# Kernel tuning notes

Hardware: AMD Instinct MI355X
Metric: run time of the kernel (lower is better)

## Reference

```python
import jax, jax.numpy as jnp
import numpy as np

NUM_HEADS = 16
D_HEAD = 128
D_MODEL = NUM_HEADS * D_HEAD  # 2048
D_LATENT = 512
F8 = jnp.float8_e4m3fn


def _q8(a):
    # emulate fp8 e4m3 numerics: quantize then compute in fp32
    return a.astype(F8).astype(jnp.float32)


def setup_inputs() -> dict:
    key = jax.random.key(0)
    ks = jax.random.split(key, 12)
    B, S = 8, 8192
    s = 0.02
    return {
        "x": jax.random.normal(ks[0], (B, S, D_MODEL), jnp.float32),
        "Wq": jax.random.normal(ks[1], (D_MODEL, D_MODEL), jnp.float32) * s,
        "bq": jnp.zeros((D_MODEL,), jnp.float32),
        "Wkv_down": jax.random.normal(ks[2], (D_MODEL, 2 * D_LATENT), jnp.float32) * s,
        "bkv_down": jnp.zeros((2 * D_LATENT,), jnp.float32),
        "Wq_down": jax.random.normal(ks[3], (D_MODEL, D_LATENT), jnp.float32) * s,
        "bq_down": jnp.zeros((D_LATENT,), jnp.float32),
        "Wkv_up": jax.random.normal(ks[4], (D_LATENT, 2 * D_MODEL), jnp.float32) * s,
        "bkv_up": jnp.zeros((2 * D_MODEL,), jnp.float32),
        "Wout": jax.random.normal(ks[5], (D_MODEL, D_MODEL), jnp.float32) * s,
        "bout": jnp.zeros((D_MODEL,), jnp.float32),
        "top_k": 2048,
    }


def reference(x, Wq, bq, Wkv_down, bkv_down, Wq_down, bq_down, Wkv_up, bkv_up, Wout, bout, top_k):
    B, S, D = x.shape
    # low-rank MQA KV cache projection: [B, S, d_latent] each
    KV = x @ Wkv_down + bkv_down
    K_down, V_down = jnp.split(KV, 2, axis=-1)

    # ---- lightning indexer (fp8-emulated fuzzy scores for the last query) ----
    q_last = x[:, -1, :]                                  # [B, D]
    q_idx = _q8(q_last) @ _q8(Wq_down) + _q8(bq_down)     # [B, d_latent]
    scores = jax.nn.relu(jnp.einsum("bl,bsl->bs", q_idx, _q8(K_down)))  # [B, S]
    _, idx = jax.lax.top_k(scores, top_k)                 # [B, k]

    # gather selected low-rank K/V tokens: [B, k, d_latent]
    K_sel = jnp.take_along_axis(K_down, idx[:, :, None], axis=1)
    V_sel = jnp.take_along_axis(V_down, idx[:, :, None], axis=1)

    # up-project to full width and split heads: [B, k, H, d_head]
    Wk_up, Wv_up = jnp.split(Wkv_up, 2, axis=1)
    bk_up, bv_up = jnp.split(bkv_up, 2, axis=0)
    K = (K_sel @ Wk_up + bk_up).reshape(B, top_k, NUM_HEADS, D_HEAD)
    V = (V_sel @ Wv_up + bv_up).reshape(B, top_k, NUM_HEADS, D_HEAD)

    # query for the current (last) position: [B, H, d_head]
    q = (q_last @ Wq + bq).reshape(B, NUM_HEADS, D_HEAD)

    logits = jnp.einsum("bhd,bkhd->bhk", q, K) / np.float32(np.sqrt(D_HEAD))
    attn = jax.nn.softmax(logits, axis=-1)                # [B, H, k]
    o = jnp.einsum("bhk,bkhd->bhd", attn, V).reshape(B, D)
    return o @ Wout + bout                                # [B, d_model]
```

## Files before the change

kernel.cpp:

```cpp
#include <hip/hip_runtime.h>
#include <hip/hip_bf16.h>
#include <math.h>

#define B_ 8
#define S_ 8192
#define D_ 2048
#define L_ 512
#define H_ 16
#define DH_ 128
#define TOPK_ 2048
#define EXTCAP 24
#define SLOTS (TOPK_ + 64)
#define RCAP 131072
#define DELTA 6e-6f
#define QCH 32
#define QCHD (D_ / QCH)
#define PCH 8
#define PCHD (D_ / PCH)
#define VCH 8
#define VCHK (SLOTS / VCH)

typedef __attribute__((ext_vector_type(8))) short short8;
typedef __attribute__((ext_vector_type(4))) float f32x4;

__device__ __forceinline__ float q8(float x) {
  float ax = fabsf(x);
  if (!(ax >= 0.015625f)) return rintf(x * 512.0f) * 0.001953125f;
  int ee; frexpf(ax, &ee);
  float step = ldexpf(1.0f, ee - 4);
  return rintf(ldexpf(x, 4 - ee)) * step;
}

__device__ __forceinline__ float q8_midf(float v, float* qflip, float* dist) {
  float av = fabsf(v);
  float step, u;
  if (!(av >= 0.015625f)) { step = 0.001953125f; u = v * 512.0f; }
  else { int ee; frexpf(av, &ee); step = ldexpf(1.0f, ee - 4); u = ldexpf(v, 4 - ee); }
  float m = rintf(u);
  float f = u - m;
  *dist = (0.5f - fabsf(f)) * step;
  float sgn = (f >= 0.0f) ? 1.0f : -1.0f;
  *qflip = (m + sgn) * step;
  return m * step;
}

__device__ __forceinline__ float b2f(unsigned u) {
  return __uint_as_float(u << 16);
}

__device__ __forceinline__ ushort bfr(float x) {
  unsigned u = __float_as_uint(x);
  return (ushort)((u + 0x7FFFu + ((u >> 16) & 1u)) >> 16);
}
__device__ __forceinline__ float uf(ushort h) {
  return __uint_as_float(((unsigned)h) << 16);
}
__device__ __forceinline__ void split3(float x, ushort& h, ushort& m, ushort& l) {
  h = bfr(x); float r = x - uf(h);
  m = bfr(r); float r2 = r - uf(m);
  l = bfr(r2);
}

__device__ __forceinline__ f32x4 mfma16(short8 a, short8 b, f32x4 c) {
  return __builtin_amdgcn_mfma_f32_16x16x32_bf16(a, b, c, 0, 0, 0);
}

#if __has_builtin(__builtin_amdgcn_global_load_lds)
#define HAS_GLL 1
__device__ __forceinline__ void gload_lds16(const void* g, void* l) {
  __builtin_amdgcn_global_load_lds(
      (const __attribute__((address_space(1))) void*)g,
      (__attribute__((address_space(3))) void*)l, 16, 0, 0);
}
#else
#define HAS_GLL 0
#endif

__global__ __launch_bounds__(256) void zero_kernel(
    int* flag, int* riskyCnt, int* extraCnt, int* cntI2O) {
  int i = blockIdx.x * 256 + threadIdx.x;
  if (i < B_ * S_) flag[i] = 0;
  if (i == 0) *riskyCnt = 0;
  if (i < B_) { extraCnt[i] = 0; cntI2O[i] = 0; }
}

__global__ __launch_bounds__(256) void wsplit_kernel(
    const float* __restrict__ W, ushort* __restrict__ Wsp) {
  const int c = blockIdx.x * 256 + threadIdx.x;
  const int kblk = blockIdx.y;
  float xe[32];
#pragma unroll
  for (int e = 0; e < 32; ++e) xe[e] = W[(long)(kblk * 32 + e) * 1024 + c];
#pragma unroll
  for (int kb = 0; kb < 4; ++kb) {
    ushort Hh[8], Mm[8], Ll[8];
#pragma unroll
    for (int e = 0; e < 8; ++e) split3(xe[kb * 8 + e], Hh[e], Mm[e], Ll[e]);
    *(short8*)&Wsp[((((long)0 * 64 + kblk) * 4 + kb) * 1024 + c) * 8] = *(short8*)Hh;
    *(short8*)&Wsp[((((long)1 * 64 + kblk) * 4 + kb) * 1024 + c) * 8] = *(short8*)Mm;
    *(short8*)&Wsp[((((long)2 * 64 + kblk) * 4 + kb) * 1024 + c) * 8] = *(short8*)Ll;
  }
}

__global__ __launch_bounds__(256) void wq8_kernel(
    const float* __restrict__ Wqd, ushort* __restrict__ Wq8) {
  const long i = ((long)blockIdx.x * 256 + threadIdx.x) * 4;
  float4 v = *(const float4*)(Wqd + i);
  ushort4 o;
  o.x = (ushort)(__float_as_uint(q8(v.x)) >> 16);
  o.y = (ushort)(__float_as_uint(q8(v.y)) >> 16);
  o.z = (ushort)(__float_as_uint(q8(v.z)) >> 16);
  o.w = (ushort)(__float_as_uint(q8(v.w)) >> 16);
  *(ushort4*)(Wq8 + i) = o;
}

#define AS_IDX(T, kb, r) ((((T)*4 + (kb)) * 128 + (r)) * 8)
#define BS_IDX(T, kb, n) ((((T)*4 + (kb)) * 128 + (n)) * 8)

template <bool QUANT>
__global__ __launch_bounds__(256, 2) void gemm_mfma(
    const float* __restrict__ X, const ushort* __restrict__ Wsp, int colbase,
    int mbase, const float* __restrict__ bias, float* __restrict__ C,
    ushort* __restrict__ Cq8, const int* __restrict__ rowmap,
    int2* __restrict__ riskyList, int* __restrict__ riskyCnt) {
  __shared__ __align__(16) ushort As[3 * 4 * 128 * 8];
  __shared__ __align__(16) ushort Bs[3 * 4 * 128 * 8];
  const int tid = threadIdx.x;
  const int m0 = (mbase + blockIdx.y) * 128;
  const int n0 = blockIdx.x * 128;
  const int ar_ = tid >> 1;
  const int kh = (tid & 1) << 4;
  const int arow = rowmap ? rowmap[m0 + ar_] : (m0 + ar_);
  const float* aptr = X + (long)arow * D_ + kh;
  const int cb = colbase + n0;

  f32x4 acc[4][4];
#pragma unroll
  for (int i = 0; i < 4; ++i)
#pragma unroll
    for (int j = 0; j < 4; ++j) acc[i][j] = (f32x4){0.f, 0.f, 0.f, 0.f};

  const int w = tid >> 6, lane = tid & 63;
  const int wm = (w & 1) * 64, wn = (w >> 1) * 64;
  const int lr = lane & 15, lq = lane >> 4;

  float4 v0 = *(const float4*)(aptr + 0);
  float4 v1 = *(const float4*)(aptr + 4);
  float4 v2 = *(const float4*)(aptr + 8);
  float4 v3 = *(const float4*)(aptr + 12);

  for (int k0 = 0; k0 < D_; k0 += 32) {
    const int kblk = k0 >> 5;

    __syncthreads();

#pragma unroll
    for (int i = 0; i < 6; ++i) {
      const int c = w * 6 + i;
      const int s = c >> 1, half = c & 1;
      const int T = s >> 2, kb = s & 3;
      const ushort* g = Wsp + ((((long)T * 64 + kblk) * 4 + kb) * 1024 +
                               (long)cb + half * 64 + lane) * 8;
#if HAS_GLL
      gload_lds16(g, &Bs[(s * 128 + half * 64) * 8]);
#else
      *(short8*)&Bs[(s * 128 + half * 64 + lane) * 8] = *(const short8*)g;
#endif
    }

    {
      float xe[16] = {v0.x, v0.y, v0.z, v0.w, v1.x, v1.y, v1.z, v1.w,
                      v2.x, v2.y, v2.z, v2.w, v3.x, v3.y, v3.z, v3.w};
      const int kb0 = (tid & 1) * 2;
#pragma unroll
      for (int j8 = 0; j8 < 2; ++j8) {
        ushort Hh[8], Mm[8], Ll[8];
#pragma unroll
        for (int e = 0; e < 8; ++e) split3(xe[j8 * 8 + e], Hh[e], Mm[e], Ll[e]);
        *(short8*)&As[AS_IDX(0, kb0 + j8, ar_)] = *(short8*)Hh;
        *(short8*)&As[AS_IDX(1, kb0 + j8, ar_)] = *(short8*)Mm;
        *(short8*)&As[AS_IDX(2, kb0 + j8, ar_)] = *(short8*)Ll;
      }
    }
    if (k0 + 32 < D_) {
      v0 = *(const float4*)(aptr + k0 + 32);
      v1 = *(const float4*)(aptr + k0 + 36);
      v2 = *(const float4*)(aptr + k0 + 40);
      v3 = *(const float4*)(aptr + k0 + 44);
    }
    __syncthreads();

    short8 af[4][3];
#pragma unroll
    for (int mf = 0; mf < 4; ++mf)
#pragma unroll
      for (int T = 0; T < 3; ++T)
        af[mf][T] = *(const short8*)&As[AS_IDX(T, lq, wm + mf * 16 + lr)];
#pragma unroll
    for (int nf = 0; nf < 4; ++nf) {
      short8 bh = *(const short8*)&Bs[BS_IDX(0, lq, wn + nf * 16 + lr)];
      short8 bm = *(const short8*)&Bs[BS_IDX(1, lq, wn + nf * 16 + lr)];
      short8 bl = *(const short8*)&Bs[BS_IDX(2, lq, wn + nf * 16 + lr)];
#pragma unroll
      for (int mf = 0; mf < 4; ++mf) {
        f32x4 c = acc[mf][nf];
        c = mfma16(af[mf][0], bh, c);
        c = mfma16(af[mf][0], bm, c);
        c = mfma16(af[mf][1], bh, c);
        c = mfma16(af[mf][0], bl, c);
        c = mfma16(af[mf][2], bh, c);
        c = mfma16(af[mf][1], bm, c);
        acc[mf][nf] = c;
      }
    }
  }

#pragma unroll
  for (int nf = 0; nf < 4; ++nf) {
    const int ng = n0 + wn + nf * 16 + lr;
    const float bb = bias[ng];
#pragma unroll
    for (int mf = 0; mf < 4; ++mf) {
      const int mg = m0 + wm + mf * 16 + lq * 4;
#pragma unroll
      for (int i = 0; i < 4; ++i) {
        float v = acc[mf][nf][i] + bb;
        const long crow = (long)(mg + i);
        C[crow * L_ + ng] = v;
        if (QUANT) {
          float qflip, dist;
          float q = q8_midf(v, &qflip, &dist);
          Cq8[crow * L_ + ng] = (ushort)(__float_as_uint(q) >> 16);
          if (dist < DELTA) {
            int idx = atomicAdd(riskyCnt, 1);
            if (idx < RCAP) {
              unsigned qbits = __float_as_uint(qflip) >> 16;
              riskyList[idx] = make_int2((int)crow, (ng << 16) | (int)qbits);
            }
          }
        }
      }
    }
  }
}

__global__ __launch_bounds__(256) void qidx_part(
    const float* __restrict__ x, const ushort* __restrict__ Wq8,
    double* __restrict__ qpart) {
  __shared__ float qs[QCHD];
  const int b = blockIdx.y;
  const int c = blockIdx.x;
  const int t = threadIdx.x;
  const int d0 = c * QCHD;
  const float* xr = x + ((long)b * S_ + (S_ - 1)) * D_ + d0;
  if (t < QCHD) qs[t] = q8(xr[t]);
  __syncthreads();
  double a0 = 0.0, a1 = 0.0;
  const ushort* wr = Wq8 + (long)d0 * L_;
  for (int dd = 0; dd < QCHD; ++dd) {
    const double qv = (double)qs[dd];
    a0 += qv * (double)b2f((unsigned)wr[dd * L_ + t]);
    a1 += qv * (double)b2f((unsigned)wr[dd * L_ + t + 256]);
  }
  double* qp = qpart + ((long)b * QCH + c) * L_;
  qp[t] = a0;
  qp[t + 256] = a1;
}

__global__ __launch_bounds__(256) void qidx_reduce(
    const double* __restrict__ qpart, const float* __restrict__ bqd,
    float* __restrict__ qidx) {
  const int i = blockIdx.x * 256 + threadIdx.x;
  const int b = i >> 9, l = i & 511;
  double acc = 0.0;
  for (int c = 0; c < QCH; ++c)
    acc += qpart[((long)b * QCH + c) * L_ + l];
  qidx[i] = (float)(acc + (double)q8(bqd[l]));
}

__global__ __launch_bounds__(256) void scores_kernel(
    const ushort* __restrict__ Kq8, const float* __restrict__ qidx,
    float* __restrict__ scores) {
  __shared__ float qs[L_];
  const int m0 = blockIdx.x * 4;
  const int b = m0 >> 13;
  const int t = threadIdx.x;
  if (t < 128) ((float4*)qs)[t] = ((const float4*)(qidx + b * L_))[t];
  __syncthreads();
  const int wave = t >> 6, lane = t & 63;
  const long m = m0 + wave;
  uint4 rv = *(const uint4*)(Kq8 + m * L_ + lane * 8);
  const float* q = qs + lane * 8;
  float p = 0.f;
  p = fmaf(q[0], b2f(rv.x & 0xffffu), p);
  p = fmaf(q[1], b2f(rv.x >> 16), p);
  p = fmaf(q[2], b2f(rv.y & 0xffffu), p);
  p = fmaf(q[3], b2f(rv.y >> 16), p);
  p = fmaf(q[4], b2f(rv.z & 0xffffu), p);
  p = fmaf(q[5], b2f(rv.z >> 16), p);
  p = fmaf(q[6], b2f(rv.w & 0xffffu), p);
  p = fmaf(q[7], b2f(rv.w >> 16), p);
#pragma unroll
  for (int off = 32; off >= 1; off >>= 1) p += __shfl_xor(p, off, 64);
  if (lane == 0) scores[m] = (p > 0.f) ? p : 0.f;
}

__global__ __launch_bounds__(256) void topk_kernel(
    const float* __restrict__ scores, int* __restrict__ rowmap,
    float* __restrict__ vstarF) {
  __shared__ unsigned su[S_];
  __shared__ int red[256];
  __shared__ int cgt_sh;
  const int b = blockIdx.x, t = threadIdx.x;
  const int wave = t >> 6, lane = t & 63;
  for (int i = t; i < S_; i += 256) su[i] = __float_as_uint(scores[(long)b * S_ + i]);
  __syncthreads();
  unsigned prefix = 0u;
  for (int bit = 30; bit >= 0; --bit) {
    unsigned cand = prefix | (1u << bit);
    int c = 0;
    for (int i = t; i < S_; i += 256) c += (su[i] >= cand) ? 1 : 0;
#pragma unroll
    for (int off = 32; off >= 1; off >>= 1) c += __shfl_xor(c, off, 64);
    if (lane == 0) red[wave] = c;
    __syncthreads();
    int total = red[0] + red[1] + red[2] + red[3];
    if (total >= TOPK_) prefix = cand;
    __syncthreads();
  }
  const unsigned vstar = prefix;
  if (t == 0) vstarF[b] = __uint_as_float(vstar);
  const int c0 = t * 32;
  int cnt = 0;
  for (int i = 0; i < 32; ++i) cnt += (su[c0 + i] > vstar) ? 1 : 0;
  red[t] = cnt;
  __syncthreads();
  if (t == 0) {
    int run = 0;
    for (int i = 0; i < 256; ++i) { int c = red[i]; red[i] = run; run += c; }
    cgt_sh = run;
  }
  __syncthreads();
  int pos = red[t];
  for (int i = 0; i < 32; ++i)
    if (su[c0 + i] > vstar) rowmap[b * TOPK_ + pos++] = b * S_ + c0 + i;
  __syncthreads();
  int tcnt = 0;
  for (int i = 0; i < 32; ++i) tcnt += (su[c0 + i] == vstar) ? 1 : 0;
  red[t] = tcnt;
  __syncthreads();
  if (t == 0) {
    int run = 0;
    for (int i = 0; i < 256; ++i) { int c = red[i]; red[i] = run; run += c; }
  }
  __syncthreads();
  int tpos = cgt_sh + red[t];
  for (int i = 0; i < 32; ++i)
    if (su[c0 + i] == vstar) {
      if (tpos < TOPK_) rowmap[b * TOPK_ + tpos] = b * S_ + c0 + i;
      ++tpos;
    }
}

__global__ __launch_bounds__(256) void risky_eval(
    const int2* __restrict__ list, const int* __restrict__ riskyCnt,
    const ushort* __restrict__ Kq8, const float* __restrict__ qidx,
    const float* __restrict__ scores, const float* __restrict__ vstarF,
    int* __restrict__ flag, int* __restrict__ extraRows,
    int* __restrict__ extraCnt, int* __restrict__ cntI2O) {
  int i = blockIdx.x * 256 + threadIdx.x;
  int n = min(*riskyCnt, RCAP);
  if (i >= n) return;
  int row = list[i].x;
  int l = list[i].y >> 16;
  float qflip = b2f((unsigned)(list[i].y & 0xffff));
  int b = row >> 13;
  float qorig = b2f((unsigned)Kq8[(long)row * L_ + l]);
  float shift = qidx[b * L_ + l] * (qflip - qorig);
  float s = scores[row];
  float vs = vstarF[b];
  bool in0 = (s >= vs);
  bool in1 = (s + shift >= vs);
  if (in0 != in1) {
    if (atomicCAS(&flag[row], 0, 1) == 0) {
      if (in0) {
        atomicAdd(&cntI2O[b], 1);
      } else {
        int e = atomicAdd(&extraCnt[b], 1);
        if (e < EXTCAP) extraRows[b * EXTCAP + e] = row;
      }
    }
  }
}

__global__ __launch_bounds__(256) void counterparty_kernel(
    const float* __restrict__ scores, const int* __restrict__ rowmap,
    const float* __restrict__ vstarF, int* __restrict__ flag,
    int* __restrict__ extraRows, int* __restrict__ extraCnt,
    const int* __restrict__ cntI2O) {
  __shared__ float bv[256];
  __shared__ int bi[256];
  const int b = blockIdx.x, t = threadIdx.x;
  const float vs = vstarF[b];
  const int nA = min(extraCnt[b], EXTCAP);
  const int nD = min(cntI2O[b], EXTCAP);
  for (int pass = 0; pass < nA; ++pass) {
    float best = 3.4e38f; int besti = -1;
    for (int k = t; k < TOPK_; k += 256) {
      int r = rowmap[b * TOPK_ + k];
      if (!flag[r]) { float s = scores[r]; if (s < best) { best = s; besti = r; } }
    }
    bv[t] = best; bi[t] = besti; __syncthreads();
    for (int off = 128; off > 0; off >>= 1) {
      if (t < off && bv[t + off] < bv[t]) { bv[t] = bv[t + off]; bi[t] = bi[t + off]; }
      __syncthreads();
    }
    if (t == 0 && bi[0] >= 0) flag[bi[0]] = 1;
    __syncthreads();
  }
  for (int pass = 0; pass < nD; ++pass) {
    float best = -3.4e38f; int besti = -1;
    for (int s0 = t; s0 < S_; s0 += 256) {
      int r = b * S_ + s0;
      float s = scores[r];
      if (s < vs && !flag[r] && s > best) { best = s; besti = r; }
    }
    bv[t] = best; bi[t] = besti; __syncthreads();
    for (int off = 128; off > 0; off >>= 1) {
      if (t < off && bv[t + off] > bv[t]) { bv[t] = bv[t + off]; bi[t] = bi[t + off]; }
      __syncthreads();
    }
    if (t == 0 && bi[0] >= 0) {
      flag[bi[0]] = 1;
      int e = extraCnt[b];
      if (e < EXTCAP) { extraRows[b * EXTCAP + e] = bi[0]; extraCnt[b] = e + 1; }
    }
    __syncthreads();
  }
}

__global__ __launch_bounds__(256) void buildext_kernel(
    const int* __restrict__ rowmap, const int* __restrict__ extraRows,
    const int* __restrict__ extraCnt, const int* __restrict__ flag,
    int* __restrict__ rowmapExt, float* __restrict__ multExt) {
  const int b = blockIdx.y;
  const int k = blockIdx.x * 256 + threadIdx.x;
  if (k >= SLOTS) return;
  const int tot = min(extraCnt[b], EXTCAP);
  int row; float m;
  if (k < TOPK_) { row = rowmap[b * TOPK_ + k]; m = flag[row] ? 0.5f : 1.0f; }
  else if (k - TOPK_ < tot) { row = extraRows[b * EXTCAP + (k - TOPK_)]; m = 0.5f; }
  else { row = b * S_; m = 0.0f; }
  rowmapExt[b * SLOTS + k] = row;
  multExt[b * SLOTS + k] = m;
}

__global__ __launch_bounds__(128) void qproj_part(
    const float* __restrict__ x, const float* __restrict__ Wq,
    float* __restrict__ ppart) {
  __shared__ float xs[PCHD];
  const int b = blockIdx.y, c = blockIdx.z, t = threadIdx.x;
  const int d0 = c * PCHD;
  const float* xr = x + ((long)b * S_ + (S_ - 1)) * D_ + d0;
  xs[t] = xr[t]; xs[t + 128] = xr[t + 128];
  __syncthreads();
  const int n = blockIdx.x * 128 + t;
  float acc = 0.f;
  for (int dd = 0; dd < PCHD; ++dd)
    acc = fmaf(xs[dd], Wq[(long)(d0 + dd) * D_ + n], acc);
  ppart[((long)c * B_ + b) * D_ + n] = acc;
}

__global__ __launch_bounds__(256) void qproj_reduce(
    const float* __restrict__ ppart, const float* __restrict__ bq,
    float* __restrict__ q) {
  const int i = blockIdx.x * 256 + threadIdx.x;
  const int b = i >> 11, n = i & (D_ - 1);
  float acc = 0.f;
  for (int c = 0; c < PCH; ++c)
    acc += ppart[((long)c * B_ + b) * D_ + n];
  q[i] = acc + bq[n];
}

__global__ __launch_bounds__(256) void qt_kernel(
    const float* __restrict__ q, const float* __restrict__ Wkvu,
    const float* __restrict__ bkvu, float* __restrict__ qt,
    float* __restrict__ blog) {
  __shared__ float qh[DH_];
  __shared__ float red[DH_];
  const int h = blockIdx.x, b = blockIdx.y, t = threadIdx.x;
  if (t < DH_) qh[t] = q[b * D_ + h * DH_ + t];
  __syncthreads();
  for (int l = t; l < L_; l += 256) {
    const float* wr = Wkvu + (long)l * 4096 + h * DH_;
    float acc = 0.f;
    for (int d = 0; d < DH_; d += 4) {
      float4 w4 = *(const float4*)(wr + d);
      acc = fmaf(qh[d], w4.x, acc);
      acc = fmaf(qh[d + 1], w4.y, acc);
      acc = fmaf(qh[d + 2], w4.z, acc);
      acc = fmaf(qh[d + 3], w4.w, acc);
    }
    qt[((long)b * H_ + h) * L_ + l] = acc;
  }
  if (t < DH_) red[t] = qh[t] * bkvu[h * DH_ + t];
  __syncthreads();
  if (t == 0) {
    float s = 0.f;
    for (int i = 0; i < DH_; ++i) s += red[i];
    blog[b * H_ + h] = s;
  }
}

__global__ __launch_bounds__(256) void logits_kernel(
    const float* __restrict__ Kd, const int* __restrict__ rowmapExt,
    const float* __restrict__ qt, const float* __restrict__ blog,
    float* __restrict__ logits) {
  const int b = blockIdx.y;
  const int k = blockIdx.x * 16 + (threadIdx.x >> 4);
  const int h = threadIdx.x & 15;
  const float* kr = Kd + (long)rowmapExt[b * SLOTS + k] * L_;
  const float* qr = qt + ((long)b * H_ + h) * L_;
  float acc = 0.f;
  for (int l = 0; l < L_; l += 4) {
    float4 kv = *(const float4*)(kr + l);
    acc = fmaf(qr[l], kv.x, acc);
    acc = fmaf(qr[l + 1], kv.y, acc);
    acc = fmaf(qr[l + 2], kv.z, acc);
    acc = fmaf(qr[l + 3], kv.w, acc);
  }
  logits[((long)b * H_ + h) * SLOTS + k] =
      (acc + blog[b * H_ + h]) * 0.088388347648318447f;
}

__global__ __launch_bounds__(256) void softmax_kernel(
    float* __restrict__ logits, const float* __restrict__ multExt) {
  __shared__ float redf[4];
  __shared__ double redd[4];
  const int bh = blockIdx.x;
  const int b = bh >> 4;
  float* row = logits + (long)bh * SLOTS;
  const float* mult = multExt + b * SLOTS;
  const int t = threadIdx.x;
  const int wave = t >> 6, lane = t & 63;
  float m = -3.4e38f;
  for (int i = t; i < SLOTS; i += 256) m = fmaxf(m, row[i]);
#pragma unroll
  for (int off = 32; off >= 1; off >>= 1) m = fmaxf(m, __shfl_xor(m, off, 64));
  if (lane == 0) redf[wave] = m;
  __syncthreads();
  m = fmaxf(fmaxf(redf[0], redf[1]), fmaxf(redf[2], redf[3]));
  double s = 0.0;
  for (int i = t; i < SLOTS; i += 256) {
    float e = expf(row[i] - m) * mult[i];
    row[i] = e;
    s += (double)e;
  }
#pragma unroll
  for (int off = 32; off >= 1; off >>= 1) s += __shfl_xor(s, off, 64);
  if (lane == 0) redd[wave] = s;
  __syncthreads();
  const float inv = (float)(1.0 / (redd[0] + redd[1] + redd[2] + redd[3]));
  for (int i = t; i < SLOTS; i += 256) row[i] *= inv;
}

__global__ __launch_bounds__(256) void vt_part(
    const float* __restrict__ Vsel, const float* __restrict__ attn,
    float* __restrict__ vpart) {
  const int b = blockIdx.y, c = blockIdx.z;
  const int t = threadIdx.x;
  const int l = blockIdx.x * 64 + (t & 63);
  const int hg = t >> 6;
  float acc[4] = {0.f, 0.f, 0.f, 0.f};
  const float* ar = attn + (long)b * H_ * SLOTS;
  const int k0 = c * VCHK, k1 = k0 + VCHK;
  for (int k = k0; k < k1; ++k) {
    float v = Vsel[((long)b * SLOTS + k) * L_ + l];
#pragma unroll
    for (int a = 0; a < 4; ++a)
      acc[a] = fmaf(ar[(hg * 4 + a) * SLOTS + k], v, acc[a]);
  }
#pragma unroll
  for (int a = 0; a < 4; ++a)
    vpart[(((long)c * B_ + b) * H_ + hg * 4 + a) * L_ + l] = acc[a];
}

__global__ __launch_bounds__(256) void vt_reduce(
    const float* __restrict__ vpart, float* __restrict__ vt) {
  const int i = blockIdx.x * 256 + threadIdx.x;
  float acc = 0.f;
  for (int c = 0; c < VCH; ++c)
    acc += vpart[(long)c * (B_ * H_ * L_) + i];
  vt[i] = acc;
}

__global__ __launch_bounds__(128) void oproj_kernel(
    const float* __restrict__ vt, const float* __restrict__ Wkvu,
    const float* __restrict__ bkvu, float* __restrict__ o) {
  __shared__ float vs[L_];
  const int h = blockIdx.x, b = blockIdx.y, t = threadIdx.x;
  for (int i = t; i < L_ / 4; i += 128)
    ((float4*)vs)[i] = ((const float4*)(vt + ((long)b * H_ + h) * L_))[i];
  __syncthreads();
  const int col = h * DH_ + t;
  float acc = 0.f;
  for (int l = 0; l < L_; ++l)
    acc = fmaf(vs[l], Wkvu[(long)l * 4096 + 2048 + col], acc);
  o[b * D_ + col] = acc + bkvu[2048 + col];
}

__global__ __launch_bounds__(128) void out_part(
    const float* __restrict__ o, const float* __restrict__ Wout,
    float* __restrict__ opart) {
  __shared__ float os[PCHD];
  const int b = blockIdx.y, c = blockIdx.z, t = threadIdx.x;
  const int d0 = c * PCHD;
  const float* orr = o + (long)b * D_ + d0;
  os[t] = orr[t]; os[t + 128] = orr[t + 128];
  __syncthreads();
  const int n = blockIdx.x * 128 + t;
  float acc = 0.f;
  for (int dd = 0; dd < PCHD; ++dd)
    acc = fmaf(os[dd], Wout[(long)(d0 + dd) * D_ + n], acc);
  opart[((long)c * B_ + b) * D_ + n] = acc;
}

__global__ __launch_bounds__(256) void out_reduce(
    const float* __restrict__ opart, const float* __restrict__ bout,
    float* __restrict__ out) {
  const int i = blockIdx.x * 256 + threadIdx.x;
  const int b = i >> 11, n = i & (D_ - 1);
  float acc = 0.f;
  for (int c = 0; c < PCH; ++c)
    acc += opart[((long)c * B_ + b) * D_ + n];
  out[i] = acc + bout[n];
}

extern "C" void kernel_launch(void* const* d_in, const int* in_sizes, int n_in,
                              void* d_out, int out_size, void* d_ws, size_t ws_size,
                              hipStream_t stream) {
  const float* x    = (const float*)d_in[0];
  const float* Wq   = (const float*)d_in[1];
  const float* bq   = (const float*)d_in[2];
  const float* Wkvd = (const float*)d_in[3];
  const float* bkvd = (const float*)d_in[4];
  const float* Wqd  = (const float*)d_in[5];
  const float* bqd  = (const float*)d_in[6];
  const float* Wkvu = (const float*)d_in[7];
  const float* bkvu = (const float*)d_in[8];
  const float* Wo   = (const float*)d_in[9];
  const float* bo   = (const float*)d_in[10];
  float* out = (float*)d_out;

  char* p = (char*)d_ws;
  auto alloc = [&](size_t bytes) {
    char* r = p;
    p += (bytes + 255) & ~(size_t)255;
    return r;
  };
  float*  Kd       = (float*)alloc((size_t)B_ * S_ * L_ * 4);
  ushort* Kq8      = (ushort*)alloc((size_t)B_ * S_ * L_ * 2);
  float*  Vsel     = (float*)alloc((size_t)B_ * SLOTS * L_ * 4);
  ushort* Wsp      = (ushort*)alloc((size_t)3 * 64 * 4 * 1024 * 8 * 2);
  ushort* Wq8      = (ushort*)alloc((size_t)D_ * L_ * 2);
  double* qpart    = (double*)alloc((size_t)B_ * QCH * L_ * 8);
  float*  ppart    = (float*)alloc((size_t)PCH * B_ * D_ * 4);
  float*  opart    = (float*)alloc((size_t)PCH * B_ * D_ * 4);
  float*  vpart    = (float*)alloc((size_t)VCH * B_ * H_ * L_ * 4);
  float*  scores   = (float*)alloc((size_t)B_ * S_ * 4);
  float*  qidx     = (float*)alloc((size_t)B_ * L_ * 4);
  int*    rowmap   = (int*)alloc((size_t)B_ * TOPK_ * 4);
  int*    rowmapE  = (int*)alloc((size_t)B_ * SLOTS * 4);
  float*  multE    = (float*)alloc((size_t)B_ * SLOTS * 4);
  float*  vstarF   = (float*)alloc((size_t)B_ * 4);
  int2*   riskyL   = (int2*)alloc((size_t)RCAP * 8);
  int*    riskyCnt = (int*)alloc(256);
  int*    flagArr  = (int*)alloc((size_t)B_ * S_ * 4);
  int*    extraR   = (int*)alloc((size_t)B_ * EXTCAP * 4);
  int*    extraCnt = (int*)alloc((size_t)B_ * 4);
  int*    cntI2O   = (int*)alloc((size_t)B_ * 4);
  float*  qv       = (float*)alloc((size_t)B_ * D_ * 4);
  float*  qt       = (float*)alloc((size_t)B_ * H_ * L_ * 4);
  float*  blog     = (float*)alloc((size_t)B_ * H_ * 4);
  float*  logits   = (float*)alloc((size_t)B_ * H_ * SLOTS * 4);
  float*  vt       = (float*)alloc((size_t)B_ * H_ * L_ * 4);
  float*  ov       = (float*)alloc((size_t)B_ * D_ * 4);
  (void)ws_size; (void)in_sizes; (void)n_in; (void)out_size;

  zero_kernel<<<(B_ * S_ + 255) / 256, 256, 0, stream>>>(flagArr, riskyCnt, extraCnt, cntI2O);
  wsplit_kernel<<<dim3(4, 64), 256, 0, stream>>>(Wkvd, Wsp);
  wq8_kernel<<<(D_ * L_ / 4) / 256, 256, 0, stream>>>(Wqd, Wq8);
  gemm_mfma<true><<<dim3(4, 256), 256, 0, stream>>>(
      x, Wsp, 0, 0, bkvd, Kd, Kq8, nullptr, riskyL, riskyCnt);
  gemm_mfma<true><<<dim3(4, 256), 256, 0, stream>>>(
      x, Wsp, 0, 256, bkvd, Kd, Kq8, nullptr, riskyL, riskyCnt);
  qidx_part<<<dim3(QCH, B_), 256, 0, stream>>>(x, Wq8, qpart);
  qidx_reduce<<<(B_ * L_) / 256, 256, 0, stream>>>(qpart, bqd, qidx);
  scores_kernel<<<(B_ * S_) / 4, 256, 0, stream>>>(Kq8, qidx, scores);
  topk_kernel<<<B_, 256, 0, stream>>>(scores, rowmap, vstarF);
  risky_eval<<<RCAP / 256, 256, 0, stream>>>(riskyL, riskyCnt, Kq8, qidx, scores, vstarF,
                                             flagArr, extraR, extraCnt, cntI2O);
  counterparty_kernel<<<B_, 256, 0, stream>>>(scores, rowmap, vstarF, flagArr, extraR, extraCnt, cntI2O);
  buildext_kernel<<<dim3((SLOTS + 255) / 256, B_), 256, 0, stream>>>(rowmap, extraR, extraCnt, flagArr, rowmapE, multE);
  gemm_mfma<false><<<dim3(4, (B_ * SLOTS) / 128), 256, 0, stream>>>(
      x, Wsp, 512, 0, bkvd + 512, Vsel, nullptr, rowmapE, nullptr, nullptr);
  qproj_part<<<dim3(D_ / 128, B_, PCH), 128, 0, stream>>>(x, Wq, ppart);
  qproj_reduce<<<(B_ * D_) / 256, 256, 0, stream>>>(ppart, bq, qv);
  qt_kernel<<<dim3(H_, B_), 256, 0, stream>>>(qv, Wkvu, bkvu, qt, blog);
  logits_kernel<<<dim3(SLOTS / 16, B_), 256, 0, stream>>>(Kd, rowmapE, qt, blog, logits);
  softmax_kernel<<<B_ * H_, 256, 0, stream>>>(logits, multE);
  vt_part<<<dim3(L_ / 64, B_, VCH), 256, 0, stream>>>(Vsel, logits, vpart);
  vt_reduce<<<(B_ * H_ * L_) / 256, 256, 0, stream>>>(vpart, vt);
  oproj_kernel<<<dim3(H_, B_), 128, 0, stream>>>(vt, Wkvu, bkvu, ov);
  out_part<<<dim3(D_ / 128, B_, PCH), 128, 0, stream>>>(ov, Wo, opart);
  out_reduce<<<(B_ * D_) / 256, 256, 0, stream>>>(opart, bo, out);
}
```

Measured before the change: 1.597 ms.

## Cut V-gather GEMM to two-term split, remap blocks, register topk, split oproj

The V-selection GEMM now uses only the high/mid bf16 split terms (three MFMAs instead of six per fragment) and skips loading and storing the low term. GEMM blocks are remapped from a 1D grid so consecutive blocks land on different XCDs. topk keeps its 32 scores per thread in registers instead of shared memory. oproj splits the latent reduction across 512 threads. The reduced-precision V path lowers accuracy of the selected V projections, which may push error past tolerance.

```diff
diff --git a/kernel.cpp b/kernel.cpp
--- a/kernel.cpp
+++ b/kernel.cpp
@@ -117,17 +117,20 @@
 #define AS_IDX(T, kb, r) ((((T)*4 + (kb)) * 128 + (r)) * 8)
 #define BS_IDX(T, kb, n) ((((T)*4 + (kb)) * 128 + (n)) * 8)
 
-template <bool QUANT>
+template <bool QUANT, int NT>
 __global__ __launch_bounds__(256, 2) void gemm_mfma(
     const float* __restrict__ X, const ushort* __restrict__ Wsp, int colbase,
     int mbase, const float* __restrict__ bias, float* __restrict__ C,
     ushort* __restrict__ Cq8, const int* __restrict__ rowmap,
     int2* __restrict__ riskyList, int* __restrict__ riskyCnt) {
+  constexpr int NP = (NT == 6) ? 3 : 2;
   __shared__ __align__(16) ushort As[3 * 4 * 128 * 8];
   __shared__ __align__(16) ushort Bs[3 * 4 * 128 * 8];
   const int tid = threadIdx.x;
-  const int m0 = (mbase + blockIdx.y) * 128;
-  const int n0 = blockIdx.x * 128;
+  const int cpx = gridDim.x >> 3;
+  const int lid = (blockIdx.x & 7) * cpx + (blockIdx.x >> 3);
+  const int m0 = (mbase + (lid >> 2)) * 128;
+  const int n0 = (lid & 3) * 128;
   const int ar_ = tid >> 1;
   const int kh = (tid & 1) << 4;
   const int arow = rowmap ? rowmap[m0 + ar_] : (m0 + ar_);
@@ -154,9 +157,10 @@
 
     __syncthreads();
 
-#pragma unroll
-    for (int i = 0; i < 6; ++i) {
-      const int c = w * 6 + i;
+    constexpr int CHW = NP * 2;
+#pragma unroll
+    for (int i = 0; i < CHW; ++i) {
+      const int c = w * CHW + i;
       const int s = c >> 1, half = c & 1;
       const int T = s >> 2, kb = s & 3;
       const ushort* g = Wsp + ((((long)T * 64 + kblk) * 4 + kb) * 1024 +
@@ -179,7 +183,8 @@
         for (int e = 0; e < 8; ++e) split3(xe[j8 * 8 + e], Hh[e], Mm[e], Ll[e]);
         *(short8*)&As[AS_IDX(0, kb0 + j8, ar_)] = *(short8*)Hh;
         *(short8*)&As[AS_IDX(1, kb0 + j8, ar_)] = *(short8*)Mm;
-        *(short8*)&As[AS_IDX(2, kb0 + j8, ar_)] = *(short8*)Ll;
+        if (NP == 3)
+          *(short8*)&As[AS_IDX(2, kb0 + j8, ar_)] = *(short8*)Ll;
       }
     }
     if (k0 + 32 < D_) {
@@ -192,24 +197,29 @@
 
     short8 af[4][3];
 #pragma unroll
-    for (int mf = 0; mf < 4; ++mf)
-#pragma unroll
-      for (int T = 0; T < 3; ++T)
-        af[mf][T] = *(const short8*)&As[AS_IDX(T, lq, wm + mf * 16 + lr)];
+    for (int mf = 0; mf < 4; ++mf) {
+      af[mf][0] = *(const short8*)&As[AS_IDX(0, lq, wm + mf * 16 + lr)];
+      af[mf][1] = *(const short8*)&As[AS_IDX(1, lq, wm + mf * 16 + lr)];
+      if (NP == 3)
+        af[mf][2] = *(const short8*)&As[AS_IDX(2, lq, wm + mf * 16 + lr)];
+    }
 #pragma unroll
     for (int nf = 0; nf < 4; ++nf) {
       short8 bh = *(const short8*)&Bs[BS_IDX(0, lq, wn + nf * 16 + lr)];
       short8 bm = *(const short8*)&Bs[BS_IDX(1, lq, wn + nf * 16 + lr)];
-      short8 bl = *(const short8*)&Bs[BS_IDX(2, lq, wn + nf * 16 + lr)];
+      short8 bl;
+      if (NP == 3) bl = *(const short8*)&Bs[BS_IDX(2, lq, wn + nf * 16 + lr)];
 #pragma unroll
       for (int mf = 0; mf < 4; ++mf) {
         f32x4 c = acc[mf][nf];
         c = mfma16(af[mf][0], bh, c);
         c = mfma16(af[mf][0], bm, c);
         c = mfma16(af[mf][1], bh, c);
-        c = mfma16(af[mf][0], bl, c);
-        c = mfma16(af[mf][2], bh, c);
-        c = mfma16(af[mf][1], bm, c);
+        if (NT == 6) {
+          c = mfma16(af[mf][0], bl, c);
+          c = mfma16(af[mf][2], bh, c);
+          c = mfma16(af[mf][1], bm, c);
+        }
         acc[mf][nf] = c;
       }
     }
@@ -308,18 +318,21 @@
 __global__ __launch_bounds__(256) void topk_kernel(
     const float* __restrict__ scores, int* __restrict__ rowmap,
     float* __restrict__ vstarF) {
-  __shared__ unsigned su[S_];
   __shared__ int red[256];
   __shared__ int cgt_sh;
   const int b = blockIdx.x, t = threadIdx.x;
   const int wave = t >> 6, lane = t & 63;
-  for (int i = t; i < S_; i += 256) su[i] = __float_as_uint(scores[(long)b * S_ + i]);
-  __syncthreads();
+  const int c0 = t * 32;
+  unsigned sv[32];
+#pragma unroll
+  for (int i = 0; i < 32; ++i)
+    sv[i] = __float_as_uint(scores[(long)b * S_ + c0 + i]);
   unsigned prefix = 0u;
   for (int bit = 30; bit >= 0; --bit) {
     unsigned cand = prefix | (1u << bit);
     int c = 0;
-    for (int i = t; i < S_; i += 256) c += (su[i] >= cand) ? 1 : 0;
+#pragma unroll
+    for (int i = 0; i < 32; ++i) c += (sv[i] >= cand) ? 1 : 0;
 #pragma unroll
     for (int off = 32; off >= 1; off >>= 1) c += __shfl_xor(c, off, 64);
     if (lane == 0) red[wave] = c;
@@ -330,9 +343,9 @@
   }
   const unsigned vstar = prefix;
   if (t == 0) vstarF[b] = __uint_as_float(vstar);
-  const int c0 = t * 32;
   int cnt = 0;
-  for (int i = 0; i < 32; ++i) cnt += (su[c0 + i] > vstar) ? 1 : 0;
+#pragma unroll
+  for (int i = 0; i < 32; ++i) cnt += (sv[i] > vstar) ? 1 : 0;
   red[t] = cnt;
   __syncthreads();
   if (t == 0) {
@@ -342,11 +355,13 @@
   }
   __syncthreads();
   int pos = red[t];
+#pragma unroll
   for (int i = 0; i < 32; ++i)
-    if (su[c0 + i] > vstar) rowmap[b * TOPK_ + pos++] = b * S_ + c0 + i;
+    if (sv[i] > vstar) rowmap[b * TOPK_ + pos++] = b * S_ + c0 + i;
   __syncthreads();
   int tcnt = 0;
-  for (int i = 0; i < 32; ++i) tcnt += (su[c0 + i] == vstar) ? 1 : 0;
+#pragma unroll
+  for (int i = 0; i < 32; ++i) tcnt += (sv[i] == vstar) ? 1 : 0;
   red[t] = tcnt;
   __syncthreads();
   if (t == 0) {
@@ -355,8 +370,9 @@
   }
   __syncthreads();
   int tpos = cgt_sh + red[t];
+#pragma unroll
   for (int i = 0; i < 32; ++i)
-    if (su[c0 + i] == vstar) {
+    if (sv[i] == vstar) {
       if (tpos < TOPK_) rowmap[b * TOPK_ + tpos] = b * S_ + c0 + i;
       ++tpos;
     }
@@ -594,19 +610,27 @@
   vt[i] = acc;
 }
 
-__global__ __launch_bounds__(128) void oproj_kernel(
+__global__ __launch_bounds__(512) void oproj_kernel(
     const float* __restrict__ vt, const float* __restrict__ Wkvu,
     const float* __restrict__ bkvu, float* __restrict__ o) {
   __shared__ float vs[L_];
+  __shared__ float part[4][DH_];
   const int h = blockIdx.x, b = blockIdx.y, t = threadIdx.x;
-  for (int i = t; i < L_ / 4; i += 128)
-    ((float4*)vs)[i] = ((const float4*)(vt + ((long)b * H_ + h) * L_))[i];
-  __syncthreads();
-  const int col = h * DH_ + t;
+  if (t < 128)
+    ((float4*)vs)[t] = ((const float4*)(vt + ((long)b * H_ + h) * L_))[t];
+  __syncthreads();
+  const int lc = t >> 7;
+  const int ct = t & 127;
+  const int col = h * DH_ + ct;
   float acc = 0.f;
-  for (int l = 0; l < L_; ++l)
+  const int l0 = lc * 128;
+  for (int l = l0; l < l0 + 128; ++l)
     acc = fmaf(vs[l], Wkvu[(long)l * 4096 + 2048 + col], acc);
-  o[b * D_ + col] = acc + bkvu[2048 + col];
+  part[lc][ct] = acc;
+  __syncthreads();
+  if (lc == 0)
+    o[b * D_ + col] = ((part[0][ct] + part[1][ct]) + (part[2][ct] + part[3][ct]))
+                      + bkvu[2048 + col];
 }
 
 __global__ __launch_bounds__(128) void out_part(
@@ -690,9 +714,9 @@
   zero_kernel<<<(B_ * S_ + 255) / 256, 256, 0, stream>>>(flagArr, riskyCnt, extraCnt, cntI2O);
   wsplit_kernel<<<dim3(4, 64), 256, 0, stream>>>(Wkvd, Wsp);
   wq8_kernel<<<(D_ * L_ / 4) / 256, 256, 0, stream>>>(Wqd, Wq8);
-  gemm_mfma<true><<<dim3(4, 256), 256, 0, stream>>>(
+  gemm_mfma<true, 6><<<1024, 256, 0, stream>>>(
       x, Wsp, 0, 0, bkvd, Kd, Kq8, nullptr, riskyL, riskyCnt);
-  gemm_mfma<true><<<dim3(4, 256), 256, 0, stream>>>(
+  gemm_mfma<true, 6><<<1024, 256, 0, stream>>>(
       x, Wsp, 0, 256, bkvd, Kd, Kq8, nullptr, riskyL, riskyCnt);
   qidx_part<<<dim3(QCH, B_), 256, 0, stream>>>(x, Wq8, qpart);
   qidx_reduce<<<(B_ * L_) / 256, 256, 0, stream>>>(qpart, bqd, qidx);
@@ -702,7 +726,7 @@
                                              flagArr, extraR, extraCnt, cntI2O);
   counterparty_kernel<<<B_, 256, 0, stream>>>(scores, rowmap, vstarF, flagArr, extraR, extraCnt, cntI2O);
   buildext_kernel<<<dim3((SLOTS + 255) / 256, B_), 256, 0, stream>>>(rowmap, extraR, extraCnt, flagArr, rowmapE, multE);
-  gemm_mfma<false><<<dim3(4, (B_ * SLOTS) / 128), 256, 0, stream>>>(
+  gemm_mfma<false, 3><<<528, 256, 0, stream>>>(
       x, Wsp, 512, 0, bkvd + 512, Vsel, nullptr, rowmapE, nullptr, nullptr);
   qproj_part<<<dim3(D_ / 128, B_, PCH), 128, 0, stream>>>(x, Wq, ppart);
   qproj_reduce<<<(B_ * D_) / 256, 256, 0, stream>>>(ppart, bq, qv);
@@ -711,7 +735,7 @@
   softmax_kernel<<<B_ * H_, 256, 0, stream>>>(logits, multE);
   vt_part<<<dim3(L_ / 64, B_, VCH), 256, 0, stream>>>(Vsel, logits, vpart);
   vt_reduce<<<(B_ * H_ * L_) / 256, 256, 0, stream>>>(vpart, vt);
-  oproj_kernel<<<dim3(H_, B_), 128, 0, stream>>>(vt, Wkvu, bkvu, ov);
+  oproj_kernel<<<dim3(H_, B_), 512, 0, stream>>>(vt, Wkvu, bkvu, ov);
   out_part<<<dim3(D_ / 128, B_, PCH), 128, 0, stream>>>(ov, Wo, opart);
   out_reduce<<<(B_ * D_) / 256, 256, 0, stream>>>(opart, bo, out);
 }
```

Result: faster. 1.433 ms (-10.3%).
